# Performance work log

Hardware: AMD Instinct MI355X
Metric: run time of the kernel (lower is better)

## Reference

```python
import jax, jax.numpy as jnp
import numpy as np

N = 100000      # nodes
E = 1600000     # edges (before self-loops)
NFEAT = 256
NHID = 16
HEADS = 8
NCLASS = 16
NEG_SLOPE = 0.2  # PyG GATConv default


def setup_inputs() -> dict:
    key = jax.random.key(0)
    ks = jax.random.split(key, 11)
    s = 0.1
    return {
        "x": jax.random.normal(ks[0], (N, NFEAT), jnp.float32),
        "edge_index": jax.random.randint(ks[1], (2, E), 0, N, jnp.int32),
        # layer 1 params (lin_src weight [H*C, F], att [H, C], bias [H*C])
        "W1": jax.random.normal(ks[2], (HEADS * NHID, NFEAT), jnp.float32) * s,
        "att_src1": jax.random.normal(ks[3], (HEADS, NHID), jnp.float32) * s,
        "att_dst1": jax.random.normal(ks[4], (HEADS, NHID), jnp.float32) * s,
        "b1": jax.random.normal(ks[5], (HEADS * NHID,), jnp.float32) * s,
        # layer 2 params (heads=1, concat=False)
        "W2": jax.random.normal(ks[6], (NCLASS, HEADS * NHID), jnp.float32) * s,
        "att_src2": jax.random.normal(ks[7], (1, NCLASS), jnp.float32) * s,
        "att_dst2": jax.random.normal(ks[8], (1, NCLASS), jnp.float32) * s,
        "b2": jax.random.normal(ks[9], (NCLASS,), jnp.float32) * s,
    }


def _gat_conv(x, src, dst, W, att_src, att_dst, bias, heads, outc, concat):
    """PyG GATConv (eval mode, edge_attr=None, self-loops already in src/dst)."""
    n = x.shape[0]
    h = (x @ W.T).reshape(n, heads, outc)                 # [N, H, C]
    a_src = (h * att_src[None]).sum(-1)                   # [N, H]
    a_dst = (h * att_dst[None]).sum(-1)                   # [N, H]
    alpha = a_src[src] + a_dst[dst]                       # [Etot, H]
    alpha = jax.nn.leaky_relu(alpha, NEG_SLOPE)
    # segment softmax over edges grouped by destination node
    amax = jax.ops.segment_max(alpha, dst, num_segments=n)  # [N, H]
    ex = jnp.exp(alpha - amax[dst])
    denom = jax.ops.segment_sum(ex, dst, num_segments=n)    # [N, H]
    attn = ex / (denom[dst] + 1e-16)                         # [Etot, H]
    msg = h[src] * attn[:, :, None]                          # [Etot, H, C]
    out = jax.ops.segment_sum(msg, dst, num_segments=n)      # [N, H, C]
    out = out.reshape(n, heads * outc) if concat else out.mean(axis=1)
    return out + bias


def reference(x, edge_index, W1, att_src1, att_dst1, b1, W2, att_src2, att_dst2, b2):
    n = x.shape[0]
    loops = jnp.arange(n, dtype=edge_index.dtype)
    src = jnp.concatenate([edge_index[0], loops])  # add_self_loops=True
    dst = jnp.concatenate([edge_index[1], loops])
    h = _gat_conv(x, src, dst, W1, att_src1, att_dst1, b1, HEADS, NHID, True)
    h = jax.nn.elu(h)
    out = _gat_conv(h, src, dst, W2, att_src2, att_dst2, b2, 1, NCLASS, False)
    return jax.nn.log_softmax(out, axis=1)
```

## Files before the change

kernel.cpp:

```cpp
#include <hip/hip_runtime.h>
#include <hip/hip_bf16.h>
#include <stdint.h>

constexpr int N     = 100000;
constexpr int E     = 1600000;
constexpr int ETOT  = E + N;
constexpr int F     = 256;
constexpr int H     = 8;
constexpr int C     = 16;
constexpr int HC    = H * C;
constexpr int NCLS  = 16;
constexpr float NEG_SLOPE = 0.2f;

constexpr int BSHIFT = 8;
constexpr int NBUCK  = (N + 255) >> BSHIFT;
constexpr int BCAP   = 8192;
constexpr int TILE   = 16384;
constexpr int NTILE  = (ETOT + TILE - 1) / TILE;

typedef __attribute__((ext_vector_type(8))) short short8;
typedef __attribute__((ext_vector_type(4))) float f32x4;
typedef __attribute__((ext_vector_type(2))) float f32x2;
typedef __attribute__((ext_vector_type(4))) unsigned int u32x4;

__device__ inline unsigned short f2bf(float f) {
    union { float f; unsigned int u; } v{f};
    unsigned int r = v.u + 0x7FFF + ((v.u >> 16) & 1);
    return (unsigned short)(r >> 16);
}
__device__ inline float bf2f(unsigned short s) {
    union { unsigned int u; float f; } v{(unsigned int)s << 16};
    return v.f;
}
__device__ inline unsigned char f2fp8(float v) {
    return (unsigned char)(__builtin_amdgcn_cvt_pk_fp8_f32(v, v, 0, false) & 0xff);
}


__global__ __launch_bounds__(256) void k_pre(const int* __restrict__ ei,
                                             int* __restrict__ bcnt,
                                             const float* __restrict__ W1,
                                             const float* __restrict__ aws,
                                             const float* __restrict__ awd,
                                             unsigned short* __restrict__ w1x) {
    __shared__ int h[NBUCK];
    int b = blockIdx.x;
    if (b < NTILE) {
        for (int i = threadIdx.x; i < NBUCK; i += 256) h[i] = 0;
        __syncthreads();
        int t0 = b * TILE;
        int t1 = (t0 + TILE < ETOT) ? t0 + TILE : ETOT;
        for (int e = t0 + threadIdx.x; e < t1; e += 256) {
            int d = (e < E) ? ei[E + e] : (e - E);
            atomicAdd(&h[d >> BSHIFT], 1);
        }
        __syncthreads();
        for (int i = threadIdx.x; i < NBUCK; i += 256) {
            int c = h[i];
            if (c) atomicAdd(&bcnt[i], c);
        }
    } else if (b < NTILE + 128) {
        int i = (b - NTILE) * 256 + threadIdx.x;
        if (i < HC * F) w1x[i] = f2bf(W1[i]);
    } else {
        int r = b - NTILE - 128;
        int k = threadIdx.x;
        int hh = r & 7;
        const float* aw = (r < 8) ? aws : awd;
        float acc = 0.f;
#pragma unroll
        for (int c = 0; c < 16; ++c)
            acc += aw[hh * 16 + c] * W1[(size_t)(hh * 16 + c) * F + k];
        w1x[(size_t)(128 + r) * F + k] = f2bf(acc);
    }
}

__global__ void k_bscan(const int* __restrict__ bcnt, int* __restrict__ boff,
                        int* __restrict__ bcur, int* __restrict__ off) {
    __shared__ int s[512];
    int tid = threadIdx.x;
    int v = (tid < NBUCK) ? bcnt[tid] : 0;
    s[tid] = v; __syncthreads();
    for (int ofs = 1; ofs < 512; ofs <<= 1) {
        int t = (tid >= ofs) ? s[tid - ofs] : 0;
        __syncthreads();
        s[tid] += t;
        __syncthreads();
    }
    if (tid < NBUCK) { int ex = s[tid] - v; boff[tid] = ex; bcur[tid] = ex; }
    if (tid == 0) off[N] = ETOT;
}


__global__ __launch_bounds__(512) void k_mid(const int* __restrict__ ei,
                                             int* __restrict__ bcur,
                                             unsigned int* __restrict__ pairs,
                                             const float* __restrict__ x,
                                             const unsigned short* __restrict__ w1x,
                                             unsigned char* __restrict__ h1f,
                                             float* __restrict__ as1,
                                             float* __restrict__ ad1) {
    __shared__ char smem[65536];
    if (blockIdx.x < NTILE) {
        int* h    = (int*)smem;
        int* base = h + NBUCK;
        int t0 = blockIdx.x * TILE;
        int t1 = (t0 + TILE < ETOT) ? t0 + TILE : ETOT;
        for (int i = threadIdx.x; i < NBUCK; i += 512) h[i] = 0;
        __syncthreads();
        for (int e = t0 + threadIdx.x; e < t1; e += 512) {
            int d = (e < E) ? ei[E + e] : (e - E);
            atomicAdd(&h[d >> BSHIFT], 1);
        }
        __syncthreads();
        for (int i = threadIdx.x; i < NBUCK; i += 512) {
            int c = h[i];
            base[i] = c ? atomicAdd(&bcur[i], c) : 0;
        }
        __syncthreads();
        for (int i = threadIdx.x; i < NBUCK; i += 512) h[i] = 0;
        __syncthreads();
        for (int e = t0 + threadIdx.x; e < t1; e += 512) {
            int s, d;
            if (e < E) { s = ei[e]; d = ei[E + e]; } else { s = e - E; d = s; }
            int b = d >> BSHIFT;
            int r = atomicAdd(&h[b], 1);
            pairs[base[b] + r] = ((unsigned)s << 8) | (unsigned)(d & 255);
        }
        return;
    }
    unsigned short* Ws = (unsigned short*)smem;
    int bid = blockIdx.x - NTILE;
    for (int i = threadIdx.x; i < 4096; i += 512) {
        int row = i >> 5;
        int c16 = i & 31;
        u32x4 v = ((const u32x4*)w1x)[i];
        int byte = row * 512 + ((c16 * 16) ^ ((row & 7) << 4));
        *((u32x4*)((char*)Ws + byte)) = v;
    }
    __syncthreads();

    int wid = threadIdx.x >> 6, lane = threadIdx.x & 63;
    int r16 = lane & 15, g = lane >> 4;
    int m = bid * 128 + wid * 16 + r16;
    int mc = (m < N) ? m : (N - 1);
    const float* xr = x + (size_t)mc * F;
    const unsigned short* wext = w1x + (size_t)(128 + r16) * F;

    f32x4 acc[9];
#pragma unroll
    for (int nf = 0; nf < 9; ++nf) acc[nf] = (f32x4){0.f, 0.f, 0.f, 0.f};

#pragma unroll
    for (int kk = 0; kk < 8; ++kk) {
        f32x4 a0 = *((const f32x4*)(xr + kk * 32 + g * 8));
        f32x4 a1 = *((const f32x4*)(xr + kk * 32 + g * 8 + 4));
        short8 af;
#pragma unroll
        for (int j = 0; j < 4; ++j) {
            af[j]     = (short)f2bf(a0[j]);
            af[4 + j] = (short)f2bf(a1[j]);
        }
        int kbyte = kk * 64 + g * 16;
#pragma unroll
        for (int nf = 0; nf < 8; ++nf) {
            int row = nf * 16 + r16;
            int byte = row * 512 + (kbyte ^ ((row & 7) << 4));
            short8 bf = *((const short8*)((const char*)Ws + byte));
            acc[nf] = __builtin_amdgcn_mfma_f32_16x16x32_bf16(af, bf, acc[nf], 0, 0, 0);
        }
        short8 bfx = *((const short8*)(wext + kk * 32 + g * 8));
        acc[8] = __builtin_amdgcn_mfma_f32_16x16x32_bf16(af, bfx, acc[8], 0, 0, 0);
    }

    int orow = bid * 128 + wid * 16 + g * 4;
#pragma unroll
    for (int j = 0; j < 4; ++j) {
        int rr = orow + j;
        if (rr >= N) continue;
        unsigned char* dst = h1f + (size_t)rr * HC + r16;
#pragma unroll
        for (int nf = 0; nf < 8; ++nf) dst[nf * 16] = f2fp8(acc[nf][j]);
        float v = acc[8][j];
        if (r16 < 8) as1[rr * 8 + r16] = v;
        else         ad1[rr * 8 + (r16 - 8)] = v;
    }
}


__global__ __launch_bounds__(256) void k_bsort(const unsigned int* __restrict__ pairs,
                                               const int* __restrict__ bcnt,
                                               const int* __restrict__ boff,
                                               int* __restrict__ csr,
                                               int* __restrict__ off) {
    __shared__ int srcs[BCAP];
    __shared__ unsigned char dl[BCAP];
    __shared__ int hist[256];
    __shared__ int sc[256];
    int b = blockIdx.x;
    int nb = bcnt[b]; if (nb > BCAP) nb = BCAP;
    int base = boff[b];
    int dbase = b << BSHIFT;
    int ndst = (N - dbase < 256) ? (N - dbase) : 256;
    int tid = threadIdx.x;

    for (int i = tid; i < nb; i += 256) {
        unsigned int p = pairs[base + i];
        srcs[i] = (int)(p >> 8);
        dl[i] = (unsigned char)(p & 255);
    }
    hist[tid] = 0;
    __syncthreads();
    for (int i = tid; i < nb; i += 256) atomicAdd(&hist[dl[i]], 1);
    __syncthreads();
    int v = hist[tid];
    sc[tid] = v;
    __syncthreads();
    for (int ofs = 1; ofs < 256; ofs <<= 1) {
        int t = (tid >= ofs) ? sc[tid - ofs] : 0;
        __syncthreads();
        sc[tid] += t;
        __syncthreads();
    }
    int lo = sc[tid] - v;
    if (tid < ndst) off[dbase + tid] = base + lo;
    hist[tid] = lo;
    __syncthreads();
    for (int i = tid; i < nb; i += 256) {
        int r = atomicAdd(&hist[dl[i]], 1);
        csr[base + r] = srcs[i];
    }
}


__global__ __launch_bounds__(256) void k_agg1(const int* __restrict__ off,
                                              const int* __restrict__ csr,
                                              const unsigned int* __restrict__ h1w,
                                              const float* __restrict__ as1,
                                              const float* __restrict__ ad1,
                                              const float* __restrict__ b1,
                                              const float* __restrict__ W2,
                                              const float* __restrict__ aw_s2,
                                              const float* __restrict__ aw_d2,
                                              unsigned short* __restrict__ h2b,
                                              float* __restrict__ as2,
                                              float* __restrict__ ad2) {
    __shared__ float W2s[128 * 17];
    for (int i = threadIdx.x; i < HC * NCLS; i += 256) {
        int j = i >> 7, k = i & 127;
        int c8 = k >> 3, q = k & 7;
        W2s[(q * 16 + c8) * 17 + j] = W2[i];
    }
    __syncthreads();

    int w = threadIdx.x >> 6, l = threadIdx.x & 63;
    int n = blockIdx.x * 4 + w;
    if (n >= N) return;
    int g  = l >> 4;
    int c8 = l & 15;
    int hh = c8 >> 1;
    unsigned int wb = (unsigned int)(c8 * 2);
    int e0 = off[n], e1 = off[n + 1];
    int deg = e1 - e0;
    float adst = ad1[n * 8 + hh];
    float den = 0.f;
    float acc[8] = {0.f, 0.f, 0.f, 0.f, 0.f, 0.f, 0.f, 0.f};

    int eb = 0;
    for (; eb + 8 <= deg; eb += 8) {
        int sA = csr[e0 + eb + g];
        int sB = csr[e0 + eb + 4 + g];
        float avA = as1[sA * 8 + hh];
        float avB = as1[sB * 8 + hh];
        uint2 vA = *((const uint2*)(h1w + ((unsigned int)sA << 5) + wb));
        uint2 vB = *((const uint2*)(h1w + ((unsigned int)sB << 5) + wb));
        float aA = avA + adst; aA = fmaxf(aA, aA * NEG_SLOPE);
        float aB = avB + adst; aB = fmaxf(aB, aB * NEG_SLOPE);
        float wA = __expf(aA), wB = __expf(aB);
        den += wA + wB;
        f32x2 a01 = __builtin_amdgcn_cvt_pk_f32_fp8(vA.x, false);
        f32x2 a23 = __builtin_amdgcn_cvt_pk_f32_fp8(vA.x, true);
        f32x2 a45 = __builtin_amdgcn_cvt_pk_f32_fp8(vA.y, false);
        f32x2 a67 = __builtin_amdgcn_cvt_pk_f32_fp8(vA.y, true);
        f32x2 b01 = __builtin_amdgcn_cvt_pk_f32_fp8(vB.x, false);
        f32x2 b23 = __builtin_amdgcn_cvt_pk_f32_fp8(vB.x, true);
        f32x2 b45 = __builtin_amdgcn_cvt_pk_f32_fp8(vB.y, false);
        f32x2 b67 = __builtin_amdgcn_cvt_pk_f32_fp8(vB.y, true);
        acc[0] += wA * a01[0] + wB * b01[0];
        acc[1] += wA * a01[1] + wB * b01[1];
        acc[2] += wA * a23[0] + wB * b23[0];
        acc[3] += wA * a23[1] + wB * b23[1];
        acc[4] += wA * a45[0] + wB * b45[0];
        acc[5] += wA * a45[1] + wB * b45[1];
        acc[6] += wA * a67[0] + wB * b67[0];
        acc[7] += wA * a67[1] + wB * b67[1];
    }
    for (; eb < deg; eb += 4) {
        int slot = eb + g;
        bool ok = slot < deg;
        int s = csr[e0 + (ok ? slot : 0)];
        float aval = as1[s * 8 + hh];
        uint2 v = *((const uint2*)(h1w + ((unsigned int)s << 5) + wb));
        float al = aval + adst; al = fmaxf(al, al * NEG_SLOPE);
        float wt = ok ? __expf(al) : 0.f;
        den += wt;
        f32x2 a01 = __builtin_amdgcn_cvt_pk_f32_fp8(v.x, false);
        f32x2 a23 = __builtin_amdgcn_cvt_pk_f32_fp8(v.x, true);
        f32x2 a45 = __builtin_amdgcn_cvt_pk_f32_fp8(v.y, false);
        f32x2 a67 = __builtin_amdgcn_cvt_pk_f32_fp8(v.y, true);
        acc[0] += wt * a01[0];
        acc[1] += wt * a01[1];
        acc[2] += wt * a23[0];
        acc[3] += wt * a23[1];
        acc[4] += wt * a45[0];
        acc[5] += wt * a45[1];
        acc[6] += wt * a67[0];
        acc[7] += wt * a67[1];
    }
#pragma unroll
    for (int q = 0; q < 8; ++q) {
        acc[q] += __shfl_xor(acc[q], 16, 64);
        acc[q] += __shfl_xor(acc[q], 32, 64);
    }
    den += __shfl_xor(den, 16, 64);
    den += __shfl_xor(den, 32, 64);

    float inv = 1.f / (den + 1e-16f);
    float v8[8];
#pragma unroll
    for (int q = 0; q < 8; ++q) {
        float v = acc[q] * inv + b1[c8 * 8 + q];
        v8[q] = (v > 0.f) ? v : (__expf(v) - 1.f);
    }
    float p0 = 0.f, p1 = 0.f, p2 = 0.f, p3 = 0.f;
#pragma unroll
    for (int q = 0; q < 8; ++q) {
        const float* wr = &W2s[(q * 16 + c8) * 17 + g * 4];
        p0 += v8[q] * wr[0];
        p1 += v8[q] * wr[1];
        p2 += v8[q] * wr[2];
        p3 += v8[q] * wr[3];
    }
#pragma unroll
    for (int msk = 8; msk >= 1; msk >>= 1) {
        p0 += __shfl_xor(p0, msk, 64);
        p1 += __shfl_xor(p1, msk, 64);
        p2 += __shfl_xor(p2, msk, 64);
        p3 += __shfl_xor(p3, msk, 64);
    }
    float sa = p0 * aw_s2[g * 4] + p1 * aw_s2[g * 4 + 1]
             + p2 * aw_s2[g * 4 + 2] + p3 * aw_s2[g * 4 + 3];
    float da = p0 * aw_d2[g * 4] + p1 * aw_d2[g * 4 + 1]
             + p2 * aw_d2[g * 4 + 2] + p3 * aw_d2[g * 4 + 3];
    sa += __shfl_xor(sa, 16, 64); sa += __shfl_xor(sa, 32, 64);
    da += __shfl_xor(da, 16, 64); da += __shfl_xor(da, 32, 64);
    if (l == 0) { as2[n] = sa; ad2[n] = da; }
    if (c8 < 4) {
        float h2v = p0;
        h2v = (c8 == 1) ? p1 : h2v;
        h2v = (c8 == 2) ? p2 : h2v;
        h2v = (c8 == 3) ? p3 : h2v;
        h2b[(size_t)n * NCLS + g * 4 + c8] = f2bf(h2v);
    }
}


__global__ __launch_bounds__(256) void k_agg2(const int* __restrict__ off,
                                              const int* __restrict__ csr,
                                              const float* __restrict__ as2,
                                              const float* __restrict__ ad2,
                                              const unsigned short* __restrict__ h2b,
                                              const float* __restrict__ b2,
                                              float* __restrict__ outp) {
    int gpos = threadIdx.x >> 4, c = threadIdx.x & 15;
    int n = blockIdx.x * 16 + gpos;
    if (n >= N) return;
    int e0 = off[n], e1 = off[n + 1];
    float adst = ad2[n];
    float den = 0.f, acc = 0.f;
    int e = e0;
    for (; e + 4 <= e1; e += 4) {
        int s0 = csr[e], s1 = csr[e + 1], s2 = csr[e + 2], s3 = csr[e + 3];
        float x0 = as2[s0], x1 = as2[s1], x2 = as2[s2], x3 = as2[s3];
        unsigned short m0 = h2b[s0 * NCLS + c], m1 = h2b[s1 * NCLS + c];
        unsigned short m2 = h2b[s2 * NCLS + c], m3 = h2b[s3 * NCLS + c];
        float a0 = x0 + adst; a0 = fmaxf(a0, a0 * NEG_SLOPE);
        float a1 = x1 + adst; a1 = fmaxf(a1, a1 * NEG_SLOPE);
        float a2 = x2 + adst; a2 = fmaxf(a2, a2 * NEG_SLOPE);
        float a3 = x3 + adst; a3 = fmaxf(a3, a3 * NEG_SLOPE);
        float w0 = __expf(a0), w1 = __expf(a1), w2 = __expf(a2), w3 = __expf(a3);
        den += (w0 + w1) + (w2 + w3);
        acc += w0 * bf2f(m0) + w1 * bf2f(m1) + w2 * bf2f(m2) + w3 * bf2f(m3);
    }
    for (; e < e1; ++e) {
        int s = csr[e];
        float al = as2[s] + adst;
        al = fmaxf(al, al * NEG_SLOPE);
        float wt = __expf(al);
        den += wt;
        acc += wt * bf2f(h2b[s * NCLS + c]);
    }
    float v = acc / (den + 1e-16f) + b2[c];
    float mx = v;
#pragma unroll
    for (int msk = 8; msk >= 1; msk >>= 1) mx = fmaxf(mx, __shfl_xor(mx, msk, 64));
    float ex = __expf(v - mx), se = ex;
#pragma unroll
    for (int msk = 8; msk >= 1; msk >>= 1) se += __shfl_xor(se, msk, 64);
    outp[n * NCLS + c] = v - mx - __logf(se);
}


extern "C" void kernel_launch(void* const* d_in, const int* in_sizes, int n_in,
                              void* d_out, int out_size, void* d_ws, size_t ws_size,
                              hipStream_t stream) {
    const float* x        = (const float*)d_in[0];
    const int*   ei       = (const int*)d_in[1];
    const float* W1       = (const float*)d_in[2];
    const float* att_src1 = (const float*)d_in[3];
    const float* att_dst1 = (const float*)d_in[4];
    const float* b1       = (const float*)d_in[5];
    const float* W2       = (const float*)d_in[6];
    const float* att_src2 = (const float*)d_in[7];
    const float* att_dst2 = (const float*)d_in[8];
    const float* b2       = (const float*)d_in[9];
    float* outp = (float*)d_out;

    char* p = (char*)d_ws;
    unsigned char* h1f    = (unsigned char*)p;  p += (size_t)N * HC;
    unsigned short* h2b   = (unsigned short*)p; p += (size_t)N * NCLS * 2;
    float* as1  = (float*)p; p += (size_t)N * H * 4;
    float* ad1  = (float*)p; p += (size_t)N * H * 4;
    float* as2  = (float*)p; p += (size_t)N * 4;
    float* ad2  = (float*)p; p += (size_t)N * 4;
    unsigned short* w1x = (unsigned short*)p; p += (size_t)144 * F * 2;
    unsigned int* pairs = (unsigned int*)p; p += (size_t)ETOT * 4;
    int* csr    = (int*)p;   p += (size_t)ETOT * 4;
    int* off    = (int*)p;   p += (size_t)(N + 1) * 4;
    int* bcnt   = (int*)p;   p += (size_t)NBUCK * 4;
    int* boff   = (int*)p;   p += (size_t)NBUCK * 4;
    int* bcur   = (int*)p;   p += (size_t)NBUCK * 4;

    hipMemsetAsync(bcnt, 0, (size_t)NBUCK * 4, stream);

    k_pre<<<NTILE + 128 + 16, 256, 0, stream>>>(ei, bcnt, W1, att_src1, att_dst1, w1x);
    k_bscan<<<1, 512, 0, stream>>>(bcnt, boff, bcur, off);
    k_mid<<<NTILE + (N + 127) / 128, 512, 0, stream>>>(ei, bcur, pairs,
                                                       x, w1x, h1f, as1, ad1);
    k_bsort<<<NBUCK, 256, 0, stream>>>(pairs, bcnt, boff, csr, off);

    k_agg1<<<(N + 3) / 4, 256, 0, stream>>>(off, csr, (const unsigned int*)h1f,
                                            as1, ad1, b1, W2, att_src2, att_dst2,
                                            h2b, as2, ad2);

    k_agg2<<<(N + 15) / 16, 256, 0, stream>>>(off, csr, as2, ad2, h2b, b2, outp);
}
```

Before: 214.0 us.

## Make layer-1 aggregation persistent with register-cached W2 and packed FMAs

The layer-1 aggregation kernel becomes grid-stride over nodes with a fixed grid of 4096 blocks. W2, the bias and the attention weights are loaded once per thread into registers instead of being staged through shared memory by every block. Accumulation now uses paired float2 vectors so packed FMAs can be emitted, and the bf16 output is written as one 8-byte store per group. The aim is to remove the per-block shared-memory setup and barrier and to cut instruction count, at the cost of more registers per thread (32 floats for W2), which may lower occupancy in a gather-latency-bound loop.

After: 213.9 us (median of 2 runs). About the same (-0.0%).

```diff
diff --git a/kernel.cpp b/kernel.cpp
--- a/kernel.cpp
+++ b/kernel.cpp
@@ -245,122 +245,112 @@
                                               unsigned short* __restrict__ h2b,
                                               float* __restrict__ as2,
                                               float* __restrict__ ad2) {
-    __shared__ float W2s[128 * 17];
-    for (int i = threadIdx.x; i < HC * NCLS; i += 256) {
-        int j = i >> 7, k = i & 127;
-        int c8 = k >> 3, q = k & 7;
-        W2s[(q * 16 + c8) * 17 + j] = W2[i];
-    }
-    __syncthreads();
-
     int w = threadIdx.x >> 6, l = threadIdx.x & 63;
-    int n = blockIdx.x * 4 + w;
-    if (n >= N) return;
     int g  = l >> 4;
     int c8 = l & 15;
     int hh = c8 >> 1;
     unsigned int wb = (unsigned int)(c8 * 2);
-    int e0 = off[n], e1 = off[n + 1];
-    int deg = e1 - e0;
-    float adst = ad1[n * 8 + hh];
-    float den = 0.f;
-    float acc[8] = {0.f, 0.f, 0.f, 0.f, 0.f, 0.f, 0.f, 0.f};
-
-    int eb = 0;
-    for (; eb + 8 <= deg; eb += 8) {
-        int sA = csr[e0 + eb + g];
-        int sB = csr[e0 + eb + 4 + g];
-        float avA = as1[sA * 8 + hh];
-        float avB = as1[sB * 8 + hh];
-        uint2 vA = *((const uint2*)(h1w + ((unsigned int)sA << 5) + wb));
-        uint2 vB = *((const uint2*)(h1w + ((unsigned int)sB << 5) + wb));
-        float aA = avA + adst; aA = fmaxf(aA, aA * NEG_SLOPE);
-        float aB = avB + adst; aB = fmaxf(aB, aB * NEG_SLOPE);
-        float wA = __expf(aA), wB = __expf(aB);
-        den += wA + wB;
-        f32x2 a01 = __builtin_amdgcn_cvt_pk_f32_fp8(vA.x, false);
-        f32x2 a23 = __builtin_amdgcn_cvt_pk_f32_fp8(vA.x, true);
-        f32x2 a45 = __builtin_amdgcn_cvt_pk_f32_fp8(vA.y, false);
-        f32x2 a67 = __builtin_amdgcn_cvt_pk_f32_fp8(vA.y, true);
-        f32x2 b01 = __builtin_amdgcn_cvt_pk_f32_fp8(vB.x, false);
-        f32x2 b23 = __builtin_amdgcn_cvt_pk_f32_fp8(vB.x, true);
-        f32x2 b45 = __builtin_amdgcn_cvt_pk_f32_fp8(vB.y, false);
-        f32x2 b67 = __builtin_amdgcn_cvt_pk_f32_fp8(vB.y, true);
-        acc[0] += wA * a01[0] + wB * b01[0];
-        acc[1] += wA * a01[1] + wB * b01[1];
-        acc[2] += wA * a23[0] + wB * b23[0];
-        acc[3] += wA * a23[1] + wB * b23[1];
-        acc[4] += wA * a45[0] + wB * b45[0];
-        acc[5] += wA * a45[1] + wB * b45[1];
-        acc[6] += wA * a67[0] + wB * b67[0];
-        acc[7] += wA * a67[1] + wB * b67[1];
-    }
-    for (; eb < deg; eb += 4) {
-        int slot = eb + g;
-        bool ok = slot < deg;
-        int s = csr[e0 + (ok ? slot : 0)];
-        float aval = as1[s * 8 + hh];
-        uint2 v = *((const uint2*)(h1w + ((unsigned int)s << 5) + wb));
-        float al = aval + adst; al = fmaxf(al, al * NEG_SLOPE);
-        float wt = ok ? __expf(al) : 0.f;
-        den += wt;
-        f32x2 a01 = __builtin_amdgcn_cvt_pk_f32_fp8(v.x, false);
-        f32x2 a23 = __builtin_amdgcn_cvt_pk_f32_fp8(v.x, true);
-        f32x2 a45 = __builtin_amdgcn_cvt_pk_f32_fp8(v.y, false);
-        f32x2 a67 = __builtin_amdgcn_cvt_pk_f32_fp8(v.y, true);
-        acc[0] += wt * a01[0];
-        acc[1] += wt * a01[1];
-        acc[2] += wt * a23[0];
-        acc[3] += wt * a23[1];
-        acc[4] += wt * a45[0];
-        acc[5] += wt * a45[1];
-        acc[6] += wt * a67[0];
-        acc[7] += wt * a67[1];
-    }
-#pragma unroll
-    for (int q = 0; q < 8; ++q) {
-        acc[q] += __shfl_xor(acc[q], 16, 64);
-        acc[q] += __shfl_xor(acc[q], 32, 64);
-    }
-    den += __shfl_xor(den, 16, 64);
-    den += __shfl_xor(den, 32, 64);
-
-    float inv = 1.f / (den + 1e-16f);
-    float v8[8];
-#pragma unroll
-    for (int q = 0; q < 8; ++q) {
-        float v = acc[q] * inv + b1[c8 * 8 + q];
-        v8[q] = (v > 0.f) ? v : (__expf(v) - 1.f);
-    }
-    float p0 = 0.f, p1 = 0.f, p2 = 0.f, p3 = 0.f;
-#pragma unroll
-    for (int q = 0; q < 8; ++q) {
-        const float* wr = &W2s[(q * 16 + c8) * 17 + g * 4];
-        p0 += v8[q] * wr[0];
-        p1 += v8[q] * wr[1];
-        p2 += v8[q] * wr[2];
-        p3 += v8[q] * wr[3];
-    }
-#pragma unroll
-    for (int msk = 8; msk >= 1; msk >>= 1) {
-        p0 += __shfl_xor(p0, msk, 64);
-        p1 += __shfl_xor(p1, msk, 64);
-        p2 += __shfl_xor(p2, msk, 64);
-        p3 += __shfl_xor(p3, msk, 64);
-    }
-    float sa = p0 * aw_s2[g * 4] + p1 * aw_s2[g * 4 + 1]
-             + p2 * aw_s2[g * 4 + 2] + p3 * aw_s2[g * 4 + 3];
-    float da = p0 * aw_d2[g * 4] + p1 * aw_d2[g * 4 + 1]
-             + p2 * aw_d2[g * 4 + 2] + p3 * aw_d2[g * 4 + 3];
-    sa += __shfl_xor(sa, 16, 64); sa += __shfl_xor(sa, 32, 64);
-    da += __shfl_xor(da, 16, 64); da += __shfl_xor(da, 32, 64);
-    if (l == 0) { as2[n] = sa; ad2[n] = da; }
-    if (c8 < 4) {
-        float h2v = p0;
-        h2v = (c8 == 1) ? p1 : h2v;
-        h2v = (c8 == 2) ? p2 : h2v;
-        h2v = (c8 == 3) ? p3 : h2v;
-        h2b[(size_t)n * NCLS + g * 4 + c8] = f2bf(h2v);
+
+    float w2f[32];
+#pragma unroll
+    for (int q = 0; q < 8; ++q)
+#pragma unroll
+        for (int j = 0; j < 4; ++j)
+            w2f[q * 4 + j] = W2[(size_t)(g * 4 + j) * HC + c8 * 8 + q];
+    float b1f[8];
+#pragma unroll
+    for (int q = 0; q < 8; ++q) b1f[q] = b1[c8 * 8 + q];
+    float awsf[4], awdf[4];
+#pragma unroll
+    for (int j = 0; j < 4; ++j) {
+        awsf[j] = aw_s2[g * 4 + j];
+        awdf[j] = aw_d2[g * 4 + j];
+    }
+
+    for (int n = blockIdx.x * 4 + w; n < N; n += gridDim.x * 4) {
+        int e0 = off[n], e1 = off[n + 1];
+        int deg = e1 - e0;
+        float adst = ad1[n * 8 + hh];
+        float den = 0.f;
+        f32x2 acc0 = {0.f, 0.f}, acc1 = {0.f, 0.f};
+        f32x2 acc2 = {0.f, 0.f}, acc3 = {0.f, 0.f};
+
+        int eb = 0;
+        for (; eb + 8 <= deg; eb += 8) {
+            int sA = csr[e0 + eb + g];
+            int sB = csr[e0 + eb + 4 + g];
+            float avA = as1[sA * 8 + hh];
+            float avB = as1[sB * 8 + hh];
+            uint2 vA = *((const uint2*)(h1w + ((unsigned int)sA << 5) + wb));
+            uint2 vB = *((const uint2*)(h1w + ((unsigned int)sB << 5) + wb));
+            float aA = avA + adst; aA = fmaxf(aA, aA * NEG_SLOPE);
+            float aB = avB + adst; aB = fmaxf(aB, aB * NEG_SLOPE);
+            float wA = __expf(aA), wB = __expf(aB);
+            den += wA + wB;
+            f32x2 wA2 = {wA, wA}, wB2 = {wB, wB};
+            acc0 += wA2 * __builtin_amdgcn_cvt_pk_f32_fp8(vA.x, false)
+                  + wB2 * __builtin_amdgcn_cvt_pk_f32_fp8(vB.x, false);
+            acc1 += wA2 * __builtin_amdgcn_cvt_pk_f32_fp8(vA.x, true)
+                  + wB2 * __builtin_amdgcn_cvt_pk_f32_fp8(vB.x, true);
+            acc2 += wA2 * __builtin_amdgcn_cvt_pk_f32_fp8(vA.y, false)
+                  + wB2 * __builtin_amdgcn_cvt_pk_f32_fp8(vB.y, false);
+            acc3 += wA2 * __builtin_amdgcn_cvt_pk_f32_fp8(vA.y, true)
+                  + wB2 * __builtin_amdgcn_cvt_pk_f32_fp8(vB.y, true);
+        }
+        for (; eb < deg; eb += 4) {
+            int slot = eb + g;
+            bool ok = slot < deg;
+            int s = csr[e0 + (ok ? slot : 0)];
+            float aval = as1[s * 8 + hh];
+            uint2 v = *((const uint2*)(h1w + ((unsigned int)s << 5) + wb));
+            float al = aval + adst; al = fmaxf(al, al * NEG_SLOPE);
+            float wt = ok ? __expf(al) : 0.f;
+            den += wt;
+            f32x2 wt2 = {wt, wt};
+            acc0 += wt2 * __builtin_amdgcn_cvt_pk_f32_fp8(v.x, false);
+            acc1 += wt2 * __builtin_amdgcn_cvt_pk_f32_fp8(v.x, true);
+            acc2 += wt2 * __builtin_amdgcn_cvt_pk_f32_fp8(v.y, false);
+            acc3 += wt2 * __builtin_amdgcn_cvt_pk_f32_fp8(v.y, true);
+        }
+        float acc[8] = {acc0[0], acc0[1], acc1[0], acc1[1],
+                        acc2[0], acc2[1], acc3[0], acc3[1]};
+#pragma unroll
+        for (int q = 0; q < 8; ++q) {
+            acc[q] += __shfl_xor(acc[q], 16, 64);
+            acc[q] += __shfl_xor(acc[q], 32, 64);
+        }
+        den += __shfl_xor(den, 16, 64);
+        den += __shfl_xor(den, 32, 64);
+
+        float inv = 1.f / (den + 1e-16f);
+        float p0 = 0.f, p1 = 0.f, p2 = 0.f, p3 = 0.f;
+#pragma unroll
+        for (int q = 0; q < 8; ++q) {
+            float v = acc[q] * inv + b1f[q];
+            v = (v > 0.f) ? v : (__expf(v) - 1.f);
+            p0 += v * w2f[q * 4 + 0];
+            p1 += v * w2f[q * 4 + 1];
+            p2 += v * w2f[q * 4 + 2];
+            p3 += v * w2f[q * 4 + 3];
+        }
+#pragma unroll
+        for (int msk = 8; msk >= 1; msk >>= 1) {
+            p0 += __shfl_xor(p0, msk, 64);
+            p1 += __shfl_xor(p1, msk, 64);
+            p2 += __shfl_xor(p2, msk, 64);
+            p3 += __shfl_xor(p3, msk, 64);
+        }
+        float sa = p0 * awsf[0] + p1 * awsf[1] + p2 * awsf[2] + p3 * awsf[3];
+        float da = p0 * awdf[0] + p1 * awdf[1] + p2 * awdf[2] + p3 * awdf[3];
+        sa += __shfl_xor(sa, 16, 64); sa += __shfl_xor(sa, 32, 64);
+        da += __shfl_xor(da, 16, 64); da += __shfl_xor(da, 32, 64);
+        if (l == 0) { as2[n] = sa; ad2[n] = da; }
+        if (c8 == 0) {
+            uint2 pk;
+            pk.x = ((unsigned int)f2bf(p1) << 16) | f2bf(p0);
+            pk.y = ((unsigned int)f2bf(p3) << 16) | f2bf(p2);
+            *((uint2*)(h2b + (size_t)n * NCLS + g * 4)) = pk;
+        }
     }
 }
 
@@ -449,9 +439,9 @@
                                                        x, w1x, h1f, as1, ad1);
     k_bsort<<<NBUCK, 256, 0, stream>>>(pairs, bcnt, boff, csr, off);
 
-    k_agg1<<<(N + 3) / 4, 256, 0, stream>>>(off, csr, (const unsigned int*)h1f,
-                                            as1, ad1, b1, W2, att_src2, att_dst2,
-                                            h2b, as2, ad2);
+    k_agg1<<<4096, 256, 0, stream>>>(off, csr, (const unsigned int*)h1f,
+                                     as1, ad1, b1, W2, att_src2, att_dst2,
+                                     h2b, as2, ad2);
 
     k_agg2<<<(N + 15) / 16, 256, 0, stream>>>(off, csr, as2, ad2, h2b, b2, outp);
 }
```
